# Kernel optimization log

Measured on AMD Instinct MI355X. Metric: run time of the kernel, lower is better.

Reference implementation:

```python
import jax, jax.numpy as jnp
import numpy as np

B, S, HID = 2, 2048, 1024
NH, NKV, HD = 8, 2, 256
G = NH // NKV              # kv groups (repeat factor)
ROT = 128                  # rotary_dim (partial RoPE)
EPS = 1e-6
SCALE = HD ** -0.5


def _rmsnorm(x, w, eps=EPS):
    # Qwen35RMSNorm: fp32 norm, (1 + weight) scale
    xf = x.astype(jnp.float32)
    n = xf * jax.lax.rsqrt(jnp.mean(xf * xf, axis=-1, keepdims=True) + eps)
    return (n * (1.0 + w.astype(jnp.float32))).astype(x.dtype)


def _rotate_half(x):
    h = x.shape[-1] // 2
    return jnp.concatenate([-x[..., h:], x[..., :h]], axis=-1)


def setup_inputs() -> dict:
    key = jax.random.key(0)
    ks = jax.random.split(key, 8)
    hidden_states = jax.random.normal(ks[0], (B, S, HID), jnp.float32)
    # realistic RoPE tables: freqs of dim ROT/2, duplicated -> ROT
    pos = jnp.arange(S, dtype=jnp.float32)
    inv_freq = 1.0 / (10000.0 ** (jnp.arange(0, ROT, 2, dtype=jnp.float32) / ROT))
    f = pos[:, None] * inv_freq[None, :]            # [S, ROT/2]
    emb = jnp.concatenate([f, f], axis=-1)          # [S, ROT]
    cos = jnp.broadcast_to(jnp.cos(emb)[None], (B, S, ROT)).astype(jnp.float32)
    sin = jnp.broadcast_to(jnp.sin(emb)[None], (B, S, ROT)).astype(jnp.float32)
    std = 0.02
    Wq = jax.random.normal(ks[1], (HID, NH * HD * 2), jnp.float32) * std
    Wk = jax.random.normal(ks[2], (HID, NKV * HD), jnp.float32) * std
    Wv = jax.random.normal(ks[3], (HID, NKV * HD), jnp.float32) * std
    Wo = jax.random.normal(ks[4], (NH * HD, HID), jnp.float32) * std
    q_norm_w = jax.random.normal(ks[5], (HD,), jnp.float32) * std
    k_norm_w = jax.random.normal(ks[6], (HD,), jnp.float32) * std
    return dict(hidden_states=hidden_states, cos=cos, sin=sin,
                Wq=Wq, Wk=Wk, Wv=Wv, Wo=Wo,
                q_norm_w=q_norm_w, k_norm_w=k_norm_w)


def reference(hidden_states, cos, sin, Wq, Wk, Wv, Wo, q_norm_w, k_norm_w):
    b, s, _ = hidden_states.shape
    # projections (Linear with weight stored [in, out])
    qg = (hidden_states @ Wq).reshape(b, s, NH, HD * 2)
    q, gate = qg[..., :HD], qg[..., HD:]            # [b,s,NH,HD] each
    gate = gate.reshape(b, s, NH * HD)
    q = _rmsnorm(q, q_norm_w)
    k = _rmsnorm((hidden_states @ Wk).reshape(b, s, NKV, HD), k_norm_w)
    v = (hidden_states @ Wv).reshape(b, s, NKV, HD)
    # partial RoPE on first ROT dims; cos/sin broadcast over heads
    c = cos[:, :, None, :]
    sn = sin[:, :, None, :]
    q_rot = q[..., :ROT] * c + _rotate_half(q[..., :ROT]) * sn
    k_rot = k[..., :ROT] * c + _rotate_half(k[..., :ROT]) * sn
    q = jnp.concatenate([q_rot, q[..., ROT:]], axis=-1)
    k = jnp.concatenate([k_rot, k[..., ROT:]], axis=-1)
    # GQA without materializing repeated KV: group q heads per kv head
    qr = q.reshape(b, s, NKV, G, HD)                # repeat_interleave layout
    scores = jnp.einsum('bqkgd,bskd->bkgqs', qr, k) * SCALE   # [b,NKV,G,S,S]
    mask = jnp.tril(jnp.ones((s, s), dtype=bool))
    scores = jnp.where(mask, scores, jnp.float32(-jnp.inf))
    probs = jax.nn.softmax(scores, axis=-1)
    out = jnp.einsum('bkgqs,bskd->bqkgd', probs, v).reshape(b, s, NH * HD)
    out = out * jax.nn.sigmoid(gate)
    return out @ Wo
```

## Files before the change

### kernel.cpp

```cpp
#include <hip/hip_runtime.h>
#include <cstdint>
#include <cstddef>

#define B_ 2
#define S_ 2048
#define HID_ 1024
#define NH_ 8
#define NKV_ 2
#define HD_ 256
#define ROT_ 128
#define TOK_ (B_ * S_)
#define SCALE_ 0.0625f

typedef __attribute__((ext_vector_type(8))) short s16x8;
typedef __attribute__((ext_vector_type(4))) float f32x4;

__device__ __forceinline__ float bf2f(short u) {
  unsigned t = ((unsigned)(unsigned short)u) << 16;
  float f;
  __builtin_memcpy(&f, &t, 4);
  return f;
}
__device__ __forceinline__ short f2bf(float f) {
  unsigned u;
  __builtin_memcpy(&u, &f, 4);
  u += 0x7fffu + ((u >> 16) & 1);
  return (short)(u >> 16);
}

__device__ __forceinline__ void gl16(const void* g, void* l) {
  __builtin_amdgcn_global_load_lds((const __attribute__((address_space(1))) int*)g,
                                   (__attribute__((address_space(3))) int*)l, 16, 0, 0);
}

__global__ __launch_bounds__(256) void k_cast(const float* __restrict__ in,
                                              short* __restrict__ out, int n) {
  int i = blockIdx.x * 256 + threadIdx.x;
  if (i < n) out[i] = f2bf(in[i]);
}

__global__ __launch_bounds__(256) void k_wtrans(const float* __restrict__ in,
                                                short* __restrict__ out, int R, int C) {
  __shared__ short tile[32][33];
  int tx = threadIdx.x & 31, ty = threadIdx.x >> 5;
  int r0 = blockIdx.y * 32, c0 = blockIdx.x * 32;
#pragma unroll
  for (int p = 0; p < 4; ++p)
    tile[ty + p * 8][tx] = f2bf(in[(size_t)(r0 + ty + p * 8) * C + c0 + tx]);
  __syncthreads();
#pragma unroll
  for (int p = 0; p < 4; ++p)
    out[(size_t)(c0 + ty + p * 8) * R + r0 + tx] = tile[tx][ty + p * 8];
}

__global__ __launch_bounds__(256) void k_vtrans(const short* __restrict__ kvp,
                                                short* __restrict__ Vtg) {
  __shared__ short tile[32][33];
  int bh = blockIdx.z;
  int b = bh >> 1, kvh = bh & 1;
  int s0 = blockIdx.x * 32, d0 = blockIdx.y * 32;
  int tx = threadIdx.x & 31, ty = threadIdx.x >> 5;
#pragma unroll
  for (int p = 0; p < 4; ++p) {
    int sr = ty + p * 8;
    tile[sr][tx] = kvp[(size_t)(b * S_ + s0 + sr) * 1024 + 512 + kvh * 256 + d0 + tx];
  }
  __syncthreads();
#pragma unroll
  for (int p = 0; p < 4; ++p) {
    int dr = ty + p * 8;
    Vtg[((size_t)bh * 256 + d0 + dr) * 2048 + s0 + tx] = tile[tx][dr];
  }
}

template <int OUT_BF16>
__global__ __launch_bounds__(256, 2) void k_gemm_bt(const short* __restrict__ A,
                                                    const short* __restrict__ Bt,
                                                    void* __restrict__ Cv, int M, int N,
                                                    int K) {
  extern __shared__ char smem[];
  const int tid = threadIdx.x;
  const int bm = blockIdx.y * 128, bn = blockIdx.x * 128;
  const int w = tid >> 6, lane = tid & 63, lo = lane & 15, hi = lane >> 4;
  const int wr = (w >> 1) * 64, wc = (w & 1) * 64;
  f32x4 acc[4][4] = {};

  auto stage = [&](int k0, int nb) {
#pragma unroll
    for (int rnd = 0; rnd < 4; ++rnd) {
      int i = rnd * 256 + tid;
      int row = i >> 3, c = i & 7;
      int src_col = (c ^ (row & 7)) * 8;
      gl16(&A[(size_t)(bm + row) * K + k0 + src_col], smem + (size_t)nb * 16384 + (size_t)i * 16);
      gl16(&Bt[(size_t)(bn + row) * K + k0 + src_col],
           smem + 32768 + (size_t)nb * 16384 + (size_t)i * 16);
    }
  };

  stage(0, 0);
  __syncthreads();
  int nb = 0;
  for (int k0 = 0; k0 < K; k0 += 64) {
    if (k0 + 64 < K) stage(k0 + 64, nb ^ 1);
    const short* As = (const short*)(smem + (size_t)nb * 16384);
    const short* Bs = (const short*)(smem + 32768 + (size_t)nb * 16384);
    s16x8 af[2][4], bfr[2][4];
#pragma unroll
    for (int kk = 0; kk < 2; ++kk) {
#pragma unroll
      for (int m = 0; m < 4; ++m) {
        int row = wr + m * 16 + lo;
        af[kk][m] = *(const s16x8*)&As[row * 64 + (((kk * 4 + hi) ^ (row & 7)) * 8)];
      }
#pragma unroll
      for (int n = 0; n < 4; ++n) {
        int row = wc + n * 16 + lo;
        bfr[kk][n] = *(const s16x8*)&Bs[row * 64 + (((kk * 4 + hi) ^ (row & 7)) * 8)];
      }
    }
#pragma unroll
    for (int kk = 0; kk < 2; ++kk)
#pragma unroll
      for (int m = 0; m < 4; ++m)
#pragma unroll
        for (int n = 0; n < 4; ++n)
          acc[m][n] =
              __builtin_amdgcn_mfma_f32_16x16x32_bf16(af[kk][m], bfr[kk][n], acc[m][n], 0, 0, 0);
    __syncthreads();
    nb ^= 1;
  }
#pragma unroll
  for (int m = 0; m < 4; ++m)
#pragma unroll
    for (int n = 0; n < 4; ++n)
#pragma unroll
      for (int r = 0; r < 4; ++r) {
        int row = bm + wr + m * 16 + hi * 4 + r;
        int col = bn + wc + n * 16 + lo;
        if (OUT_BF16)
          ((short*)Cv)[(size_t)row * N + col] = f2bf(acc[m][n][r]);
        else
          ((float*)Cv)[(size_t)row * N + col] = acc[m][n][r];
      }
}

template <int OUT_BF16>
__global__ __launch_bounds__(512, 1) void k_gemm256(const short* __restrict__ A,
                                                    const short* __restrict__ Bt,
                                                    void* __restrict__ Cv, int M, int N,
                                                    int K) {
  extern __shared__ char smem[];
  const int tid = threadIdx.x;
  const int bm = blockIdx.y * 256, bn = blockIdx.x * 256;
  const int w = tid >> 6, lane = tid & 63, lo = lane & 15, hi = lane >> 4;
  const int wr = (w >> 2) * 128, wc = (w & 3) * 64;
  f32x4 acc[8][4] = {};

  auto stage = [&](int k0, int nb) {
#pragma unroll
    for (int rnd = 0; rnd < 4; ++rnd) {
      int i = rnd * 512 + tid;
      int row = i >> 3, c = i & 7;
      int src_col = (c ^ (row & 7)) * 8;
      gl16(&A[(size_t)(bm + row) * K + k0 + src_col], smem + (size_t)nb * 32768 + (size_t)i * 16);
      gl16(&Bt[(size_t)(bn + row) * K + k0 + src_col],
           smem + 65536 + (size_t)nb * 32768 + (size_t)i * 16);
    }
  };

  stage(0, 0);
  __syncthreads();
  int nb = 0;
  for (int k0 = 0; k0 < K; k0 += 64) {
    if (k0 + 64 < K) stage(k0 + 64, nb ^ 1);
    const short* As = (const short*)(smem + (size_t)nb * 32768);
    const short* Bs = (const short*)(smem + 65536 + (size_t)nb * 32768);
#pragma unroll
    for (int kk = 0; kk < 2; ++kk) {
      s16x8 bfr[4];
#pragma unroll
      for (int n = 0; n < 4; ++n) {
        int row = wc + n * 16 + lo;
        bfr[n] = *(const s16x8*)&Bs[row * 64 + (((kk * 4 + hi) ^ (row & 7)) * 8)];
      }
#pragma unroll
      for (int g = 0; g < 2; ++g) {
        s16x8 af[4];
#pragma unroll
        for (int u = 0; u < 4; ++u) {
          int row = wr + (g * 4 + u) * 16 + lo;
          af[u] = *(const s16x8*)&As[row * 64 + (((kk * 4 + hi) ^ (row & 7)) * 8)];
        }
#pragma unroll
        for (int u = 0; u < 4; ++u)
#pragma unroll
          for (int n = 0; n < 4; ++n)
            acc[g * 4 + u][n] =
                __builtin_amdgcn_mfma_f32_16x16x32_bf16(af[u], bfr[n], acc[g * 4 + u][n], 0, 0, 0);
      }
    }
    __syncthreads();
    nb ^= 1;
  }
#pragma unroll
  for (int m = 0; m < 8; ++m)
#pragma unroll
    for (int n = 0; n < 4; ++n)
#pragma unroll
      for (int r = 0; r < 4; ++r) {
        int row = bm + wr + m * 16 + hi * 4 + r;
        int col = bn + wc + n * 16 + lo;
        if (OUT_BF16)
          ((short*)Cv)[(size_t)row * N + col] = f2bf(acc[m][n][r]);
        else
          ((float*)Cv)[(size_t)row * N + col] = acc[m][n][r];
      }
}

template <int NHEAD, int IN_ROW, int IN_HS>
__global__ __launch_bounds__(256) void k_norm_rope(const short* __restrict__ xin,
                                                   const float* __restrict__ wn,
                                                   const float* __restrict__ cosb,
                                                   const float* __restrict__ sinb,
                                                   short* __restrict__ xout) {
  int blk = blockIdx.x;
  int h = blk % NHEAD;
  int ts = blk / NHEAD;
  int d = threadIdx.x;
  float x = bf2f(xin[(size_t)ts * IN_ROW + h * IN_HS + d]);
  float ss = x * x;
#pragma unroll
  for (int m = 32; m >= 1; m >>= 1) ss += __shfl_xor(ss, m);
  __shared__ float sred[4];
  __shared__ float sn[256];
  int wid = d >> 6;
  if ((d & 63) == 0) sred[wid] = ss;
  __syncthreads();
  float tot = sred[0] + sred[1] + sred[2] + sred[3];
  float nv = x * rsqrtf(tot * (1.0f / 256.0f) + 1e-6f) * (1.0f + wn[d]);
  sn[d] = nv;
  __syncthreads();
  float o;
  if (d < 128) {
    float c = cosb[(size_t)ts * 128 + d];
    float s = sinb[(size_t)ts * 128 + d];
    o = (d < 64) ? (nv * c - sn[d + 64] * s) : (nv * c + sn[d - 64] * s);
  } else {
    o = nv;
  }
  xout[(size_t)blk * 256 + d] = f2bf(o);
}

#define ATTN_LDS 131072
__global__ __launch_bounds__(512, 1) void k_attn(const short* __restrict__ qb,
                                                 const short* __restrict__ kb,
                                                 const short* __restrict__ Vtg,
                                                 short* __restrict__ Po,
                                                 float* __restrict__ Pm,
                                                 float* __restrict__ Pl) {
  extern __shared__ char smem[];
  short* KbufS = (short*)smem;
  short* VbufS = (short*)(smem + 65536);

  const int raw = blockIdx.x;
  const int xcd = raw & 7, slot = raw >> 3;
  const int p = xcd >> 1, side = xcd & 1;
  const int id = side * 32 + slot;
  const int hgi = id & 3, j = id >> 2;
  const int b = p >> 1, kvh = p & 1, h = kvh * 4 + hgi;
  const int tid = threadIdx.x;
  const int w = tid >> 6, lane = tid & 63, lo = lane & 15, hi = lane >> 4;
  const int swz = lo & 7;

  const short* kbase = kb + ((size_t)(b * S_) * NKV_ + kvh) * HD_;
  const short* vbase = Vtg + (size_t)(b * 2 + kvh) * 256 * 2048;

  auto stage = [&](int kv0, int nb) {
#pragma unroll
    for (int rnd = 0; rnd < 4; ++rnd) {
      int i = rnd * 512 + tid;
      {
        int row = i >> 5, c = i & 31;
        const short* src = kbase + (size_t)(kv0 + row) * 512 + ((c ^ (row & 7)) * 8);
        gl16(src, smem + (size_t)nb * 32768 + (size_t)i * 16);
      }
      {
        int row = i >> 3, c = i & 7;
        const short* src = vbase + (size_t)row * 2048 + kv0 + ((c ^ (row & 7)) * 8);
        gl16(src, smem + 65536 + (size_t)nb * 32768 + (size_t)i * 16);
      }
    }
  };

#pragma unroll 1
  for (int part = 0; part < 2; ++part) {
    const int qt = part ? (15 - j) : j;
    const int q0 = qt * 128;
    const int t_begin = part ? (qt + 1) : 0;
    const int t_end = part ? (2 * qt + 2) : (qt + 1);

    s16x8 qf[8];
    {
      size_t base = ((size_t)((b * S_ + q0 + w * 16 + lo) * NH_) + h) * HD_;
#pragma unroll
      for (int t = 0; t < 8; ++t) qf[t] = *(const s16x8*)&qb[base + t * 32 + hi * 8];
    }
    f32x4 acc[16];
#pragma unroll
    for (int t = 0; t < 16; ++t) acc[t] = (f32x4){0.f, 0.f, 0.f, 0.f};
    float m_run = -1e30f, l_run = 0.f;
    const int qrow = q0 + w * 16 + lo;

    stage(t_begin * 64, 0);
    __syncthreads();

    int n = 0;
#pragma unroll 1
    for (int it = t_begin; it < t_end; ++it) {
      const int kv0 = it * 64;
      if (it + 1 < t_end) stage(kv0 + 64, n ^ 1);

      const short* Kb = KbufS + n * 16384;
      const short* Vb = VbufS + n * 16384;

      f32x4 sacc[4] = {};
#pragma unroll
      for (int nt = 0; nt < 4; ++nt) {
        s16x8 kf[8];
#pragma unroll
        for (int t = 0; t < 8; ++t)
          kf[t] = *(const s16x8*)&Kb[(nt * 16 + lo) * 256 + (((t * 4 + hi) ^ swz) * 8)];
#pragma unroll
        for (int t = 0; t < 8; ++t)
          sacc[nt] = __builtin_amdgcn_mfma_f32_16x16x32_bf16(kf[t], qf[t], sacc[nt], 0, 0, 0);
      }

      float pv[4][4];
      float mx = -1e30f;
#pragma unroll
      for (int nt = 0; nt < 4; ++nt)
#pragma unroll
        for (int r = 0; r < 4; ++r) {
          int kv = kv0 + nt * 16 + hi * 4 + r;
          float s = sacc[nt][r] * SCALE_;
          if (kv > qrow) s = -1e30f;
          pv[nt][r] = s;
          mx = fmaxf(mx, s);
        }
      mx = fmaxf(mx, __shfl_xor(mx, 16));
      mx = fmaxf(mx, __shfl_xor(mx, 32));
      if (!__all(mx <= m_run + 8.f)) {
        float mnew = fmaxf(m_run, mx);
        float fs = __expf(m_run - mnew);
        m_run = mnew;
        l_run *= fs;
        float f0 = __shfl(fs, 4 * hi + 0);
        float f1 = __shfl(fs, 4 * hi + 1);
        float f2 = __shfl(fs, 4 * hi + 2);
        float f3 = __shfl(fs, 4 * hi + 3);
#pragma unroll
        for (int t = 0; t < 16; ++t) {
          acc[t][0] *= f0;
          acc[t][1] *= f1;
          acc[t][2] *= f2;
          acc[t][3] *= f3;
        }
      }
      float rs = 0.f;
#pragma unroll
      for (int nt = 0; nt < 4; ++nt)
#pragma unroll
        for (int r = 0; r < 4; ++r) {
          pv[nt][r] = __expf(pv[nt][r] - m_run);
          rs += pv[nt][r];
        }
      rs += __shfl_xor(rs, 16);
      rs += __shfl_xor(rs, 32);
      l_run += rs;

      int pk0[4], pk1[4];
#pragma unroll
      for (int nt = 0; nt < 4; ++nt) {
        asm("v_cvt_pk_bf16_f32 %0, %1, %2" : "=v"(pk0[nt]) : "v"(pv[nt][0]), "v"(pv[nt][1]));
        asm("v_cvt_pk_bf16_f32 %0, %1, %2" : "=v"(pk1[nt]) : "v"(pv[nt][2]), "v"(pv[nt][3]));
      }

#pragma unroll
      for (int ks = 0; ks < 2; ++ks) {
        int pw[4];
#pragma unroll
        for (int dw = 0; dw < 4; ++dw) {
          int srcl = (2 * (hi & 1) + (dw >> 1)) * 16 + lo;
          int vA = __shfl((dw & 1) ? pk1[2 * ks] : pk0[2 * ks], srcl);
          int vB = __shfl((dw & 1) ? pk1[2 * ks + 1] : pk0[2 * ks + 1], srcl);
          pw[dw] = (hi & 2) ? vB : vA;
        }
        s16x8 pa;
        __builtin_memcpy(&pa, pw, 16);
#pragma unroll
        for (int g = 0; g < 2; ++g) {
          s16x8 vf[8];
#pragma unroll
          for (int u = 0; u < 8; ++u) {
            int t = g * 8 + u;
            vf[u] = *(const s16x8*)&Vb[(t * 16 + lo) * 64 + (((ks * 4 + hi) ^ swz) * 8)];
          }
#pragma unroll
          for (int u = 0; u < 8; ++u) {
            int t = g * 8 + u;
            acc[t] = __builtin_amdgcn_mfma_f32_16x16x32_bf16(pa, vf[u], acc[t], 0, 0, 0);
          }
        }
      }
      __syncthreads();
      n ^= 1;
    }

    const int tile2 = ((b * 8 + h) * 16 + qt) * 2 + part;
    float linv[4];
#pragma unroll
    for (int r = 0; r < 4; ++r) {
      float lr = __shfl(l_run, 4 * hi + r);
      linv[r] = lr > 0.f ? 1.0f / lr : 0.f;
    }
#pragma unroll
    for (int t = 0; t < 16; ++t)
#pragma unroll
      for (int r = 0; r < 4; ++r)
        Po[(size_t)tile2 * 32768 + (w * 16 + hi * 4 + r) * 256 + t * 16 + lo] =
            f2bf(acc[t][r] * linv[r]);
    if (hi == 0) {
      Pm[tile2 * 128 + w * 16 + lo] = m_run;
      Pl[tile2 * 128 + w * 16 + lo] = l_run;
    }
  }
}

__global__ __launch_bounds__(256) void k_merge(const short* __restrict__ Po,
                                               const float* __restrict__ Pm,
                                               const float* __restrict__ Pl,
                                               const short* __restrict__ qg,
                                               short* __restrict__ og) {
  const int tile = blockIdx.x >> 4, rc = blockIdx.x & 15;
  const int b = tile >> 7, h = (tile >> 4) & 7, qt = tile & 15;
  const int t = threadIdx.x;
  const int r = t >> 5, rl = rc * 8 + r, c0 = (t & 31) * 8;
  const int row = qt * 128 + rl;
  const size_t base = (size_t)tile * 2 * 32768;
  s16x8 o0 = *(const s16x8*)&Po[base + rl * 256 + c0];
  s16x8 o1 = *(const s16x8*)&Po[base + 32768 + rl * 256 + c0];
  float m0 = Pm[tile * 256 + rl], m1 = Pm[tile * 256 + 128 + rl];
  float l0 = Pl[tile * 256 + rl], l1 = Pl[tile * 256 + 128 + rl];
  float mm = fmaxf(m0, m1);
  float w0 = l0 * __expf(m0 - mm), w1 = l1 * __expf(m1 - mm);
  float inv = 1.0f / (w0 + w1);
  s16x8 gv = *(const s16x8*)&qg[(size_t)(b * S_ + row) * 4096 + h * 512 + 256 + c0];
  s16x8 outv;
#pragma unroll
  for (int jj = 0; jj < 8; ++jj) {
    float o = (w0 * bf2f(o0[jj]) + w1 * bf2f(o1[jj])) * inv;
    float g = bf2f(gv[jj]);
    float sg = 1.0f / (1.0f + __expf(-g));
    outv[jj] = f2bf(o * sg);
  }
  *(s16x8*)&og[(size_t)(b * S_ + row) * 2048 + h * 256 + c0] = outv;
}

extern "C" void kernel_launch(void* const* d_in, const int* in_sizes, int n_in, void* d_out,
                              int out_size, void* d_ws, size_t ws_size, hipStream_t stream) {
  const float* hidden = (const float*)d_in[0];
  const float* cosb = (const float*)d_in[1];
  const float* sinb = (const float*)d_in[2];
  const float* Wq = (const float*)d_in[3];
  const float* Wk = (const float*)d_in[4];
  const float* Wv = (const float*)d_in[5];
  const float* Wo = (const float*)d_in[6];
  const float* qw = (const float*)d_in[7];
  const float* kw = (const float*)d_in[8];
  float* out = (float*)d_out;

  char* ws = (char*)d_ws;
  size_t off = 0;
  auto alloc = [&](size_t bytes) {
    void* p = ws + off;
    off += (bytes + 255) & ~(size_t)255;
    return p;
  };
  short* hb = (short*)alloc((size_t)TOK_ * HID_ * 2);
  short* WqT = (short*)alloc((size_t)4096 * 1024 * 2);
  short* kvT = (short*)alloc((size_t)1024 * 1024 * 2);
  short* WoT = (short*)alloc((size_t)1024 * 2048 * 2);
  short* qg = (short*)alloc((size_t)TOK_ * 4096 * 2);
  short* kvp = (short*)alloc((size_t)TOK_ * 1024 * 2);
  short* qb = (short*)alloc((size_t)TOK_ * 2048 * 2);
  short* kb = (short*)alloc((size_t)TOK_ * 512 * 2);
  short* og = (short*)alloc((size_t)TOK_ * 2048 * 2);
  short* Po = (short*)alloc((size_t)512 * 32768 * 2);
  float* Pm = (float*)alloc((size_t)512 * 128 * 4);
  float* Pl = (float*)alloc((size_t)512 * 128 * 4);
  short* Vtg = WqT;
  (void)ws_size;
  (void)in_sizes;
  (void)n_in;
  (void)out_size;

  hipFuncSetAttribute((const void*)k_attn, hipFuncAttributeMaxDynamicSharedMemorySize,
                      ATTN_LDS);
  hipFuncSetAttribute((const void*)k_gemm256<1>, hipFuncAttributeMaxDynamicSharedMemorySize,
                      131072);
  hipFuncSetAttribute((const void*)k_gemm_bt<1>, hipFuncAttributeMaxDynamicSharedMemorySize,
                      65536);
  hipFuncSetAttribute((const void*)k_gemm_bt<0>, hipFuncAttributeMaxDynamicSharedMemorySize,
                      65536);

  k_cast<<<(TOK_ * HID_ + 255) / 256, 256, 0, stream>>>(hidden, hb, TOK_ * HID_);
  k_wtrans<<<dim3(4096 / 32, 1024 / 32), 256, 0, stream>>>(Wq, WqT, 1024, 4096);
  k_wtrans<<<dim3(512 / 32, 1024 / 32), 256, 0, stream>>>(Wk, kvT, 1024, 512);
  k_wtrans<<<dim3(512 / 32, 1024 / 32), 256, 0, stream>>>(Wv, kvT + 512 * 1024, 1024, 512);
  k_wtrans<<<dim3(1024 / 32, 2048 / 32), 256, 0, stream>>>(Wo, WoT, 2048, 1024);

  k_gemm256<1><<<dim3(16, 16), 512, 131072, stream>>>(hb, WqT, qg, 4096, 4096, 1024);
  k_gemm_bt<1><<<dim3(8, 32), 256, 65536, stream>>>(hb, kvT, kvp, 4096, 1024, 1024);

  k_norm_rope<NH_, 4096, 512><<<TOK_ * NH_, 256, 0, stream>>>(qg, qw, cosb, sinb, qb);
  k_norm_rope<NKV_, 1024, 256><<<TOK_ * NKV_, 256, 0, stream>>>(kvp, kw, cosb, sinb, kb);
  k_vtrans<<<dim3(64, 8, 4), 256, 0, stream>>>(kvp, Vtg);

  k_attn<<<256, 512, ATTN_LDS, stream>>>(qb, kb, Vtg, Po, Pm, Pl);
  k_merge<<<4096, 256, 0, stream>>>(Po, Pm, Pl, qg, og);

  k_gemm_bt<0><<<dim3(8, 32), 256, 65536, stream>>>(og, WoT, out, 4096, 1024, 2048);
}
```

Measured before the change: 207.9 us.

## Shrink Q-projection GEMM tile for two blocks per CU; prefetch attention part-1 KV

The Q/gate projection GEMM moves from a 256x256 tile with a K-step of 64 to a 128x256 tile with a K-step of 32. This cuts LDS to 48KB and allows two 512-thread blocks per CU, giving 512 blocks instead of 256 for better occupancy and wave balance. The cost is less data reuse per block and more barriers. In the attention kernel, the first KV tile of the second query part is now prefetched during the last iteration of the first part, which removes one exposed load-and-sync bubble between the two parts.

```diff
diff --git a/kernel.cpp b/kernel.cpp
--- a/kernel.cpp
+++ b/kernel.cpp
@@ -145,65 +145,62 @@
 }
 
 template <int OUT_BF16>
-__global__ __launch_bounds__(512, 1) void k_gemm256(const short* __restrict__ A,
-                                                    const short* __restrict__ Bt,
-                                                    void* __restrict__ Cv, int M, int N,
-                                                    int K) {
+__global__ __launch_bounds__(512, 2) void k_gemm1(const short* __restrict__ A,
+                                                  const short* __restrict__ Bt,
+                                                  void* __restrict__ Cv, int M, int N,
+                                                  int K) {
   extern __shared__ char smem[];
   const int tid = threadIdx.x;
-  const int bm = blockIdx.y * 256, bn = blockIdx.x * 256;
+  const int bm = blockIdx.y * 128, bn = blockIdx.x * 256;
   const int w = tid >> 6, lane = tid & 63, lo = lane & 15, hi = lane >> 4;
-  const int wr = (w >> 2) * 128, wc = (w & 3) * 64;
-  f32x4 acc[8][4] = {};
+  const int wr = (w >> 2) * 64, wc = (w & 3) * 64;
+  f32x4 acc[4][4] = {};
 
   auto stage = [&](int k0, int nb) {
-#pragma unroll
-    for (int rnd = 0; rnd < 4; ++rnd) {
+    {
+      int i = tid;
+      int row = i >> 2, c = i & 3;
+      int sc = (c ^ (row & 3)) * 8;
+      gl16(&A[(size_t)(bm + row) * K + k0 + sc], smem + (size_t)nb * 8192 + (size_t)i * 16);
+    }
+#pragma unroll
+    for (int rnd = 0; rnd < 2; ++rnd) {
       int i = rnd * 512 + tid;
-      int row = i >> 3, c = i & 7;
-      int src_col = (c ^ (row & 7)) * 8;
-      gl16(&A[(size_t)(bm + row) * K + k0 + src_col], smem + (size_t)nb * 32768 + (size_t)i * 16);
-      gl16(&Bt[(size_t)(bn + row) * K + k0 + src_col],
-           smem + 65536 + (size_t)nb * 32768 + (size_t)i * 16);
+      int row = i >> 2, c = i & 3;
+      int sc = (c ^ (row & 3)) * 8;
+      gl16(&Bt[(size_t)(bn + row) * K + k0 + sc],
+           smem + 16384 + (size_t)nb * 16384 + (size_t)i * 16);
     }
   };
 
   stage(0, 0);
   __syncthreads();
   int nb = 0;
-  for (int k0 = 0; k0 < K; k0 += 64) {
-    if (k0 + 64 < K) stage(k0 + 64, nb ^ 1);
-    const short* As = (const short*)(smem + (size_t)nb * 32768);
-    const short* Bs = (const short*)(smem + 65536 + (size_t)nb * 32768);
-#pragma unroll
-    for (int kk = 0; kk < 2; ++kk) {
-      s16x8 bfr[4];
-#pragma unroll
-      for (int n = 0; n < 4; ++n) {
-        int row = wc + n * 16 + lo;
-        bfr[n] = *(const s16x8*)&Bs[row * 64 + (((kk * 4 + hi) ^ (row & 7)) * 8)];
-      }
-#pragma unroll
-      for (int g = 0; g < 2; ++g) {
-        s16x8 af[4];
-#pragma unroll
-        for (int u = 0; u < 4; ++u) {
-          int row = wr + (g * 4 + u) * 16 + lo;
-          af[u] = *(const s16x8*)&As[row * 64 + (((kk * 4 + hi) ^ (row & 7)) * 8)];
-        }
-#pragma unroll
-        for (int u = 0; u < 4; ++u)
-#pragma unroll
-          for (int n = 0; n < 4; ++n)
-            acc[g * 4 + u][n] =
-                __builtin_amdgcn_mfma_f32_16x16x32_bf16(af[u], bfr[n], acc[g * 4 + u][n], 0, 0, 0);
-      }
-    }
+  for (int k0 = 0; k0 < K; k0 += 32) {
+    if (k0 + 32 < K) stage(k0 + 32, nb ^ 1);
+    const short* As = (const short*)(smem + (size_t)nb * 8192);
+    const short* Bs = (const short*)(smem + 16384 + (size_t)nb * 16384);
+    s16x8 af[4], bfr[4];
+#pragma unroll
+    for (int m = 0; m < 4; ++m) {
+      int row = wr + m * 16 + lo;
+      af[m] = *(const s16x8*)&As[row * 32 + ((hi ^ (row & 3)) * 8)];
+    }
+#pragma unroll
+    for (int n = 0; n < 4; ++n) {
+      int row = wc + n * 16 + lo;
+      bfr[n] = *(const s16x8*)&Bs[row * 32 + ((hi ^ (row & 3)) * 8)];
+    }
+#pragma unroll
+    for (int m = 0; m < 4; ++m)
+#pragma unroll
+      for (int n = 0; n < 4; ++n)
+        acc[m][n] = __builtin_amdgcn_mfma_f32_16x16x32_bf16(af[m], bfr[n], acc[m][n], 0, 0, 0);
     __syncthreads();
     nb ^= 1;
   }
 #pragma unroll
-  for (int m = 0; m < 8; ++m)
+  for (int m = 0; m < 4; ++m)
 #pragma unroll
     for (int n = 0; n < 4; ++n)
 #pragma unroll
@@ -292,6 +289,7 @@
     }
   };
 
+  int n = 0;
 #pragma unroll 1
   for (int part = 0; part < 2; ++part) {
     const int qt = part ? (15 - j) : j;
@@ -311,14 +309,18 @@
     float m_run = -1e30f, l_run = 0.f;
     const int qrow = q0 + w * 16 + lo;
 
-    stage(t_begin * 64, 0);
-    __syncthreads();
-
-    int n = 0;
+    if (part == 0) {
+      stage(0, 0);
+      __syncthreads();
+    }
+
 #pragma unroll 1
     for (int it = t_begin; it < t_end; ++it) {
       const int kv0 = it * 64;
-      if (it + 1 < t_end) stage(kv0 + 64, n ^ 1);
+      if (it + 1 < t_end)
+        stage(kv0 + 64, n ^ 1);
+      else if (part == 0)
+        stage((16 - j) * 64, n ^ 1);
 
       const short* Kb = KbufS + n * 16384;
       const short* Vb = VbufS + n * 16384;
@@ -506,8 +508,8 @@
 
   hipFuncSetAttribute((const void*)k_attn, hipFuncAttributeMaxDynamicSharedMemorySize,
                       ATTN_LDS);
-  hipFuncSetAttribute((const void*)k_gemm256<1>, hipFuncAttributeMaxDynamicSharedMemorySize,
-                      131072);
+  hipFuncSetAttribute((const void*)k_gemm1<1>, hipFuncAttributeMaxDynamicSharedMemorySize,
+                      49152);
   hipFuncSetAttribute((const void*)k_gemm_bt<1>, hipFuncAttributeMaxDynamicSharedMemorySize,
                       65536);
   hipFuncSetAttribute((const void*)k_gemm_bt<0>, hipFuncAttributeMaxDynamicSharedMemorySize,
@@ -519,7 +521,7 @@
   k_wtrans<<<dim3(512 / 32, 1024 / 32), 256, 0, stream>>>(Wv, kvT + 512 * 1024, 1024, 512);
   k_wtrans<<<dim3(1024 / 32, 2048 / 32), 256, 0, stream>>>(Wo, WoT, 2048, 1024);
 
-  k_gemm256<1><<<dim3(16, 16), 512, 131072, stream>>>(hb, WqT, qg, 4096, 4096, 1024);
+  k_gemm1<1><<<dim3(16, 32), 512, 49152, stream>>>(hb, WqT, qg, 4096, 4096, 1024);
   k_gemm_bt<1><<<dim3(8, 32), 256, 65536, stream>>>(hb, kvT, kvp, 4096, 1024, 1024);
 
   k_norm_rope<NH_, 4096, 512><<<TOK_ * NH_, 256, 0, stream>>>(qg, qw, cosb, sinb, qb);
```

Result: slower. 215.8 us (+3.8%).

## Split attention KV range into four chunks with smaller tiles, two blocks per CU

Applied to the files above, without the earlier changes.

Attention KV tiles shrink from 64 to 32 keys, which halves LDS use to 64KB and lets two 512-thread blocks share a CU. Each query tile's causal KV range is now split into four equal chunks instead of two, doubling the grid to 512 blocks. The next part's first tile is prefetched across the part boundary. The merge kernel now combines four partials per row, which doubles the partial-output workspace and the merge traffic, and the smaller tiles add more per-iteration sync and softmax overhead.

```diff
diff --git a/kernel.cpp b/kernel.cpp
--- a/kernel.cpp
+++ b/kernel.cpp
@@ -251,8 +251,8 @@
   xout[(size_t)blk * 256 + d] = f2bf(o);
 }
 
-#define ATTN_LDS 131072
-__global__ __launch_bounds__(512, 1) void k_attn(const short* __restrict__ qb,
+#define ATTN_LDS 65536
+__global__ __launch_bounds__(512, 2) void k_attn(const short* __restrict__ qb,
                                                  const short* __restrict__ kb,
                                                  const short* __restrict__ Vtg,
                                                  short* __restrict__ Po,
@@ -260,44 +260,48 @@
                                                  float* __restrict__ Pl) {
   extern __shared__ char smem[];
   short* KbufS = (short*)smem;
-  short* VbufS = (short*)(smem + 65536);
+  short* VbufS = (short*)(smem + 32768);
 
   const int raw = blockIdx.x;
   const int xcd = raw & 7, slot = raw >> 3;
   const int p = xcd >> 1, side = xcd & 1;
-  const int id = side * 32 + slot;
-  const int hgi = id & 3, j = id >> 2;
+  const int id = side * 64 + slot;
+  const int hgi = id & 3;
+  const int rest = id >> 2;
+  const int j = rest & 7, cq = rest >> 3;
   const int b = p >> 1, kvh = p & 1, h = kvh * 4 + hgi;
   const int tid = threadIdx.x;
   const int w = tid >> 6, lane = tid & 63, lo = lane & 15, hi = lane >> 4;
-  const int swz = lo & 7;
+  const int swz = lo & 7, swz3 = lo & 3;
 
   const short* kbase = kb + ((size_t)(b * S_) * NKV_ + kvh) * HD_;
   const short* vbase = Vtg + (size_t)(b * 2 + kvh) * 256 * 2048;
 
   auto stage = [&](int kv0, int nb) {
 #pragma unroll
-    for (int rnd = 0; rnd < 4; ++rnd) {
+    for (int rnd = 0; rnd < 2; ++rnd) {
       int i = rnd * 512 + tid;
       {
-        int row = i >> 5, c = i & 31;
-        const short* src = kbase + (size_t)(kv0 + row) * 512 + ((c ^ (row & 7)) * 8);
-        gl16(src, smem + (size_t)nb * 32768 + (size_t)i * 16);
+        int row = i >> 5, cc = i & 31;
+        gl16(kbase + (size_t)(kv0 + row) * 512 + ((cc ^ (row & 7)) * 8),
+             smem + (size_t)nb * 16384 + (size_t)i * 16);
       }
       {
-        int row = i >> 3, c = i & 7;
-        const short* src = vbase + (size_t)row * 2048 + kv0 + ((c ^ (row & 7)) * 8);
-        gl16(src, smem + 65536 + (size_t)nb * 32768 + (size_t)i * 16);
+        int row = i >> 2, cc = i & 3;
+        gl16(vbase + (size_t)row * 2048 + kv0 + ((cc ^ (row & 3)) * 8),
+             smem + 32768 + (size_t)nb * 16384 + (size_t)i * 16);
       }
     }
   };
 
+  int n = 0;
 #pragma unroll 1
   for (int part = 0; part < 2; ++part) {
     const int qt = part ? (15 - j) : j;
+    const int nQ = qt + 1;
+    const int t_begin = cq * nQ;
+    const int t_end = t_begin + nQ;
     const int q0 = qt * 128;
-    const int t_begin = part ? (qt + 1) : 0;
-    const int t_end = part ? (2 * qt + 2) : (qt + 1);
 
     s16x8 qf[8];
     {
@@ -311,21 +315,25 @@
     float m_run = -1e30f, l_run = 0.f;
     const int qrow = q0 + w * 16 + lo;
 
-    stage(t_begin * 64, 0);
-    __syncthreads();
-
-    int n = 0;
+    if (part == 0) {
+      stage(t_begin * 32, 0);
+      __syncthreads();
+    }
+
 #pragma unroll 1
     for (int it = t_begin; it < t_end; ++it) {
-      const int kv0 = it * 64;
-      if (it + 1 < t_end) stage(kv0 + 64, n ^ 1);
-
-      const short* Kb = KbufS + n * 16384;
-      const short* Vb = VbufS + n * 16384;
-
-      f32x4 sacc[4] = {};
-#pragma unroll
-      for (int nt = 0; nt < 4; ++nt) {
+      const int kv0 = it * 32;
+      if (it + 1 < t_end)
+        stage(kv0 + 32, n ^ 1);
+      else if (part == 0)
+        stage(cq * (16 - j) * 32, n ^ 1);
+
+      const short* Kb = KbufS + n * 8192;
+      const short* Vb = VbufS + n * 8192;
+
+      f32x4 sacc[2] = {};
+#pragma unroll
+      for (int nt = 0; nt < 2; ++nt) {
         s16x8 kf[8];
 #pragma unroll
         for (int t = 0; t < 8; ++t)
@@ -335,10 +343,10 @@
           sacc[nt] = __builtin_amdgcn_mfma_f32_16x16x32_bf16(kf[t], qf[t], sacc[nt], 0, 0, 0);
       }
 
-      float pv[4][4];
+      float pv[2][4];
       float mx = -1e30f;
 #pragma unroll
-      for (int nt = 0; nt < 4; ++nt)
+      for (int nt = 0; nt < 2; ++nt)
 #pragma unroll
         for (int r = 0; r < 4; ++r) {
           int kv = kv0 + nt * 16 + hi * 4 + r;
@@ -368,7 +376,7 @@
       }
       float rs = 0.f;
 #pragma unroll
-      for (int nt = 0; nt < 4; ++nt)
+      for (int nt = 0; nt < 2; ++nt)
 #pragma unroll
         for (int r = 0; r < 4; ++r) {
           pv[nt][r] = __expf(pv[nt][r] - m_run);
@@ -378,21 +386,20 @@
       rs += __shfl_xor(rs, 32);
       l_run += rs;
 
-      int pk0[4], pk1[4];
-#pragma unroll
-      for (int nt = 0; nt < 4; ++nt) {
+      int pk0[2], pk1[2];
+#pragma unroll
+      for (int nt = 0; nt < 2; ++nt) {
         asm("v_cvt_pk_bf16_f32 %0, %1, %2" : "=v"(pk0[nt]) : "v"(pv[nt][0]), "v"(pv[nt][1]));
         asm("v_cvt_pk_bf16_f32 %0, %1, %2" : "=v"(pk1[nt]) : "v"(pv[nt][2]), "v"(pv[nt][3]));
       }
 
-#pragma unroll
-      for (int ks = 0; ks < 2; ++ks) {
+      {
         int pw[4];
 #pragma unroll
         for (int dw = 0; dw < 4; ++dw) {
           int srcl = (2 * (hi & 1) + (dw >> 1)) * 16 + lo;
-          int vA = __shfl((dw & 1) ? pk1[2 * ks] : pk0[2 * ks], srcl);
-          int vB = __shfl((dw & 1) ? pk1[2 * ks + 1] : pk0[2 * ks + 1], srcl);
+          int vA = __shfl((dw & 1) ? pk1[0] : pk0[0], srcl);
+          int vB = __shfl((dw & 1) ? pk1[1] : pk0[1], srcl);
           pw[dw] = (hi & 2) ? vB : vA;
         }
         s16x8 pa;
@@ -403,7 +410,7 @@
 #pragma unroll
           for (int u = 0; u < 8; ++u) {
             int t = g * 8 + u;
-            vf[u] = *(const s16x8*)&Vb[(t * 16 + lo) * 64 + (((ks * 4 + hi) ^ swz) * 8)];
+            vf[u] = *(const s16x8*)&Vb[(t * 16 + lo) * 32 + ((hi ^ swz3) * 8)];
           }
 #pragma unroll
           for (int u = 0; u < 8; ++u) {
@@ -416,7 +423,7 @@
       n ^= 1;
     }
 
-    const int tile2 = ((b * 8 + h) * 16 + qt) * 2 + part;
+    const int tile4 = (((b * 8 + h) * 16 + qt) << 2) + cq;
     float linv[4];
 #pragma unroll
     for (int r = 0; r < 4; ++r) {
@@ -427,11 +434,11 @@
     for (int t = 0; t < 16; ++t)
 #pragma unroll
       for (int r = 0; r < 4; ++r)
-        Po[(size_t)tile2 * 32768 + (w * 16 + hi * 4 + r) * 256 + t * 16 + lo] =
+        Po[(size_t)tile4 * 32768 + (w * 16 + hi * 4 + r) * 256 + t * 16 + lo] =
             f2bf(acc[t][r] * linv[r]);
     if (hi == 0) {
-      Pm[tile2 * 128 + w * 16 + lo] = m_run;
-      Pl[tile2 * 128 + w * 16 + lo] = l_run;
+      Pm[tile4 * 128 + w * 16 + lo] = m_run;
+      Pl[tile4 * 128 + w * 16 + lo] = l_run;
     }
   }
 }
@@ -446,19 +453,32 @@
   const int t = threadIdx.x;
   const int r = t >> 5, rl = rc * 8 + r, c0 = (t & 31) * 8;
   const int row = qt * 128 + rl;
-  const size_t base = (size_t)tile * 2 * 32768;
-  s16x8 o0 = *(const s16x8*)&Po[base + rl * 256 + c0];
-  s16x8 o1 = *(const s16x8*)&Po[base + 32768 + rl * 256 + c0];
-  float m0 = Pm[tile * 256 + rl], m1 = Pm[tile * 256 + 128 + rl];
-  float l0 = Pl[tile * 256 + rl], l1 = Pl[tile * 256 + 128 + rl];
-  float mm = fmaxf(m0, m1);
-  float w0 = l0 * __expf(m0 - mm), w1 = l1 * __expf(m1 - mm);
-  float inv = 1.0f / (w0 + w1);
+  s16x8 ov[4];
+  float mv[4], lv[4];
+  float mm = -1e30f;
+#pragma unroll
+  for (int i = 0; i < 4; ++i) {
+    int t4 = tile * 4 + i;
+    ov[i] = *(const s16x8*)&Po[(size_t)t4 * 32768 + rl * 256 + c0];
+    mv[i] = Pm[t4 * 128 + rl];
+    lv[i] = Pl[t4 * 128 + rl];
+    mm = fmaxf(mm, mv[i]);
+  }
+  float wsum = 0.f, wv[4];
+#pragma unroll
+  for (int i = 0; i < 4; ++i) {
+    wv[i] = lv[i] * __expf(mv[i] - mm);
+    wsum += wv[i];
+  }
+  float inv = 1.0f / wsum;
   s16x8 gv = *(const s16x8*)&qg[(size_t)(b * S_ + row) * 4096 + h * 512 + 256 + c0];
   s16x8 outv;
 #pragma unroll
   for (int jj = 0; jj < 8; ++jj) {
-    float o = (w0 * bf2f(o0[jj]) + w1 * bf2f(o1[jj])) * inv;
+    float o = 0.f;
+#pragma unroll
+    for (int i = 0; i < 4; ++i) o += wv[i] * bf2f(ov[i][jj]);
+    o *= inv;
     float g = bf2f(gv[jj]);
     float sg = 1.0f / (1.0f + __expf(-g));
     outv[jj] = f2bf(o * sg);
@@ -495,9 +515,9 @@
   short* qb = (short*)alloc((size_t)TOK_ * 2048 * 2);
   short* kb = (short*)alloc((size_t)TOK_ * 512 * 2);
   short* og = (short*)alloc((size_t)TOK_ * 2048 * 2);
-  short* Po = (short*)alloc((size_t)512 * 32768 * 2);
-  float* Pm = (float*)alloc((size_t)512 * 128 * 4);
-  float* Pl = (float*)alloc((size_t)512 * 128 * 4);
+  short* Po = (short*)alloc((size_t)1024 * 32768 * 2);
+  float* Pm = (float*)alloc((size_t)1024 * 128 * 4);
+  float* Pl = (float*)alloc((size_t)1024 * 128 * 4);
   short* Vtg = WqT;
   (void)ws_size;
   (void)in_sizes;
@@ -526,7 +546,7 @@
   k_norm_rope<NKV_, 1024, 256><<<TOK_ * NKV_, 256, 0, stream>>>(kvp, kw, cosb, sinb, kb);
   k_vtrans<<<dim3(64, 8, 4), 256, 0, stream>>>(kvp, Vtg);
 
-  k_attn<<<256, 512, ATTN_LDS, stream>>>(qb, kb, Vtg, Po, Pm, Pl);
+  k_attn<<<512, 512, ATTN_LDS, stream>>>(qb, kb, Vtg, Po, Pm, Pl);
   k_merge<<<4096, 256, 0, stream>>>(Po, Pm, Pl, qg, og);
 
   k_gemm_bt<0><<<dim3(8, 32), 256, 65536, stream>>>(og, WoT, out, 4096, 1024, 2048);
```

New measurement: 232.3 us. 11.8% more time.
